# Kernel optimization log

Measured on AMD Instinct MI355X. Metric: run time of the kernel, lower is better.

Reference implementation:

```python
import jax, jax.numpy as jnp
import numpy as np

NUM_GROUPS = 32
EPS = 1e-6


def group_norm(x, gamma, beta):
    # x: [b, c, h, w]
    b, c, h, w = x.shape
    g = NUM_GROUPS
    xg = x.reshape(b, g, c // g, h, w)
    mean = xg.mean(axis=(2, 3, 4), keepdims=True)
    var = xg.var(axis=(2, 3, 4), keepdims=True)
    xn = ((xg - mean) * jax.lax.rsqrt(var + EPS)).reshape(b, c, h, w)
    return xn * gamma[None, :, None, None] + beta[None, :, None, None]


def conv1x1(x, w, b):
    # x: [b, c, h, w], w: [out_c, in_c], b: [out_c]
    return jnp.einsum('bchw,oc->bohw', x, w) + b[None, :, None, None]


def setup_inputs() -> dict:
    key = jax.random.key(0)
    ks = jax.random.split(key, 11)
    B, C, H, W = 4, 512, 64, 64
    s = 1.0 / np.sqrt(C)
    inp = {
        'x': jax.random.normal(ks[0], (B, C, H, W), dtype=jnp.float32),
        'gn_gamma': jnp.ones((C,), dtype=jnp.float32),
        'gn_beta': jnp.zeros((C,), dtype=jnp.float32),
        'wq': jax.random.normal(ks[1], (C, C), dtype=jnp.float32) * s,
        'bq': jax.random.normal(ks[2], (C,), dtype=jnp.float32) * 0.01,
        'wk': jax.random.normal(ks[3], (C, C), dtype=jnp.float32) * s,
        'bk': jax.random.normal(ks[4], (C,), dtype=jnp.float32) * 0.01,
        'wv': jax.random.normal(ks[5], (C, C), dtype=jnp.float32) * s,
        'bv': jax.random.normal(ks[6], (C,), dtype=jnp.float32) * 0.01,
        'wo': jax.random.normal(ks[7], (C, C), dtype=jnp.float32) * s,
        'bo': jax.random.normal(ks[8], (C,), dtype=jnp.float32) * 0.01,
    }
    return inp


def reference(x, gn_gamma, gn_beta, wq, bq, wk, bk, wv, bv, wo, bo):
    b, c, h, w = x.shape
    h_ = group_norm(x, gn_gamma, gn_beta)
    q = conv1x1(h_, wq, bq).reshape(b, c, h * w)  # [b, c, n]
    k = conv1x1(h_, wk, bk).reshape(b, c, h * w)
    v = conv1x1(h_, wv, bv).reshape(b, c, h * w)
    scale = jnp.asarray(c, x.dtype) ** -0.5
    # attn[b, i, j] = softmax_j(q_i . k_j * scale)
    attn = jax.nn.softmax(jnp.einsum('bci,bcj->bij', q, k) * scale, axis=-1)
    # A[b, c, i] = sum_j attn[b, i, j] * v[b, c, j]
    A = jnp.einsum('bij,bcj->bci', attn, v).reshape(b, c, h, w)
    A = conv1x1(A, wo, bo)
    # NOTE: the original module multiplies (not adds) the input by the attention output
    return x * A
```

## Files before the change

### kernel.cpp

```cpp
#include <hip/hip_runtime.h>
#include <hip/hip_bf16.h>
#include <stdint.h>

typedef __bf16 bf16x8 __attribute__((ext_vector_type(8)));
typedef __bf16 bf16x4 __attribute__((ext_vector_type(4)));
typedef float f32x4 __attribute__((ext_vector_type(4)));

__device__ __forceinline__ void gload_lds16(const __bf16* g, __bf16* l) {
  __builtin_amdgcn_global_load_lds(
      (const __attribute__((address_space(1))) void*)g,
      (__attribute__((address_space(3))) void*)l, 16, 0, 0);
}

__global__ __launch_bounds__(256) void cvt4_kernel(const float* __restrict__ s0,
                                                   const float* __restrict__ s1,
                                                   const float* __restrict__ s2,
                                                   const float* __restrict__ s3,
                                                   __bf16* __restrict__ dst) {
  int i = blockIdx.x * 256 + threadIdx.x;
  const float* srcs[4] = {s0, s1, s2, s3};
  int m = i >> 18;
  dst[i] = (__bf16)srcs[m][i & 262143];
}

__global__ __launch_bounds__(256) void biascat_kernel(const float* __restrict__ bq,
                                                      const float* __restrict__ bk,
                                                      float* __restrict__ bqk) {
  int i = blockIdx.x * 256 + threadIdx.x;
  bqk[i] = (i < 512) ? bq[i] : bk[i - 512];
}

__global__ __launch_bounds__(256) void gn1a_kernel(const float* __restrict__ x,
                                                   __bf16* __restrict__ xbf,
                                                   float2* __restrict__ part) {
  const int tid = threadIdx.x;
  const int s = blockIdx.x & 7;
  const int g = (blockIdx.x >> 3) & 31;
  const int b = blockIdx.x >> 8;
  const size_t base4 = (((size_t)b * 512 + g * 16) * 4096 + s * 8192) >> 2;
  const float4* x4 = (const float4*)x;
  bf16x4* o4 = (bf16x4*)xbf;

  float s1 = 0.f, s2 = 0.f;
#pragma unroll
  for (int j = 0; j < 8; ++j) {
    float4 t = x4[base4 + tid + j * 256];
    s1 += t.x + t.y + t.z + t.w;
    s2 += t.x * t.x + t.y * t.y + t.z * t.z + t.w * t.w;
    bf16x4 o;
    o[0] = (__bf16)t.x; o[1] = (__bf16)t.y; o[2] = (__bf16)t.z; o[3] = (__bf16)t.w;
    o4[base4 + tid + j * 256] = o;
  }
#pragma unroll
  for (int off = 32; off; off >>= 1) {
    s1 += __shfl_xor(s1, off);
    s2 += __shfl_xor(s2, off);
  }
  __shared__ float r1[4], r2[4];
  if ((tid & 63) == 0) { r1[tid >> 6] = s1; r2[tid >> 6] = s2; }
  __syncthreads();
  if (tid == 0)
    part[blockIdx.x] = float2{r1[0] + r1[1] + r1[2] + r1[3],
                              r2[0] + r2[1] + r2[2] + r2[3]};
}

__global__ __launch_bounds__(512) void gn1b_kernel(const float2* __restrict__ part,
                                                   const float* __restrict__ gamma,
                                                   const float* __restrict__ beta,
                                                   float2* __restrict__ gmbt) {
  const int b = blockIdx.x;
  const int t = threadIdx.x;
  __shared__ float sm[32], si[32];
  if (t < 32) {
    float s1 = 0.f, s2 = 0.f;
#pragma unroll
    for (int j = 0; j < 8; ++j) {
      float2 p = part[(b * 32 + t) * 8 + j];
      s1 += p.x; s2 += p.y;
    }
    const float mean = s1 * (1.f / 65536.f);
    const float var = s2 * (1.f / 65536.f) - mean * mean;
    sm[t] = mean;
    si[t] = rsqrtf(var + 1e-6f);
  }
  __syncthreads();
  const int g = t >> 4;
  const float gm = gamma[t] * si[g];
  gmbt[b * 512 + t] = float2{gm, beta[t] - sm[g] * gm};
}

__global__ __launch_bounds__(256) void gn2_kernel(const __bf16* __restrict__ xbf,
                                                  const float2* __restrict__ gmbt,
                                                  __bf16* __restrict__ hnT) {
  const int b = blockIdx.z;
  const int c0 = blockIdx.y * 64;
  const int n0 = blockIdx.x * 64;
  const int t = threadIdx.x;
  __shared__ __bf16 tile[64][72];

  {
    const int row = t >> 2;
    const int col = (t & 3) * 16;
    const __bf16* src = xbf + ((size_t)(b * 512 + c0 + row)) * 4096 + n0 + col;
    bf16x8 u0 = *(const bf16x8*)src;
    bf16x8 u1 = *(const bf16x8*)(src + 8);
    *(bf16x8*)&tile[row][col] = u0;
    *(bf16x8*)&tile[row][col + 8] = u1;
  }
  __syncthreads();
  {
    const int nrow = t >> 2;
    const int cc = (t & 3) * 16;
    bf16x8 o0, o1;
#pragma unroll
    for (int j = 0; j < 16; ++j) {
      const int c = c0 + cc + j;
      float2 s = gmbt[b * 512 + c];
      float val = (float)tile[cc + j][nrow] * s.x + s.y;
      if (j < 8) o0[j] = (__bf16)val; else o1[j - 8] = (__bf16)val;
    }
    __bf16* dst = hnT + ((size_t)b * 4096 + n0 + nrow) * 512 + c0 + cc;
    *(bf16x8*)dst = o0;
    *(bf16x8*)(dst + 8) = o1;
  }
}

__global__ __launch_bounds__(256) void softmax_bf16_kernel(__bf16* __restrict__ S) {
  const int N = 4096;
  __bf16* rp = S + (size_t)blockIdx.x * N;
  const int tid = threadIdx.x;
  bf16x8 v0 = ((const bf16x8*)rp)[tid * 2];
  bf16x8 v1 = ((const bf16x8*)rp)[tid * 2 + 1];
  float f[16];
#pragma unroll
  for (int i = 0; i < 8; ++i) { f[i] = (float)v0[i]; f[8 + i] = (float)v1[i]; }

  float mx = -1e30f;
#pragma unroll
  for (int i = 0; i < 16; ++i) mx = fmaxf(mx, f[i]);
#pragma unroll
  for (int off = 32; off; off >>= 1) mx = fmaxf(mx, __shfl_xor(mx, off));
  __shared__ float redm[4];
  if ((tid & 63) == 0) redm[tid >> 6] = mx;
  __syncthreads();
  mx = fmaxf(fmaxf(redm[0], redm[1]), fmaxf(redm[2], redm[3]));

  float sum = 0.f;
#pragma unroll
  for (int i = 0; i < 16; ++i) {
    f[i] = __expf(f[i] - mx);
    sum += f[i];
  }
#pragma unroll
  for (int off = 32; off; off >>= 1) sum += __shfl_xor(sum, off);
  __shared__ float reds[4];
  if ((tid & 63) == 0) reds[tid >> 6] = sum;
  __syncthreads();
  sum = reds[0] + reds[1] + reds[2] + reds[3];
  const float invs = 1.0f / sum;

  bf16x8 o0, o1;
#pragma unroll
  for (int i = 0; i < 8; ++i) {
    o0[i] = (__bf16)(f[i] * invs);
    o1[i] = (__bf16)(f[8 + i] * invs);
  }
  ((bf16x8*)rp)[tid * 2] = o0;
  ((bf16x8*)rp)[tid * 2 + 1] = o1;
}

template <int EPI, int BIAS>
__global__ __launch_bounds__(256) void gemm_lds_kernel(
    const __bf16* __restrict__ A, int lda, long long sA,
    const __bf16* __restrict__ Bm, int ldb, long long sB,
    void* __restrict__ Out, int ldo, long long sO,
    const float* __restrict__ bias, const __bf16* __restrict__ xmul,
    long long sX, float scale, int K) {
  __shared__ __bf16 sTa[2][128 * 32];
  __shared__ __bf16 sTb[2][128 * 32];

  const int gx = gridDim.x, gxy = gx * gridDim.y;
  const int nwg = gxy * gridDim.z;
  int bid = blockIdx.x + gx * blockIdx.y + gxy * blockIdx.z;
  if ((nwg & 7) == 0) bid = (bid & 7) * (nwg >> 3) + (bid >> 3);
  const int bz = bid / gxy;
  const int rem = bid - bz * gxy;
  const int by = rem / gx;
  const int bx = rem - by * gx;

  const int tid = threadIdx.x;
  const int lane = tid & 63;
  const int wid = tid >> 6;
  const int wr = wid >> 1, wc = wid & 1;
  const int tm0 = by * 128, tn0 = bx * 128;
  const int lr = lane & 15, lk = (lane >> 4) * 8;

  const int ch0 = wid * 2;
  const int srow = lane >> 2;
  const int scol = (lane & 3) * 8;
  const __bf16* gA0 = A + (size_t)bz * sA + (size_t)(tm0 + ch0 * 16 + srow) * lda + scol;
  const __bf16* gB0 = Bm + (size_t)bz * sB + (size_t)(tn0 + ch0 * 16 + srow) * ldb + scol;
  const size_t stepA = (size_t)16 * lda, stepB = (size_t)16 * ldb;

  f32x4 acc[4][4];
#pragma unroll
  for (int i = 0; i < 4; ++i)
#pragma unroll
    for (int j = 0; j < 4; ++j) acc[i][j] = f32x4{0.f, 0.f, 0.f, 0.f};

  const int T = K >> 5;
  gload_lds16(gA0, &sTa[0][ch0 * 512]);
  gload_lds16(gA0 + stepA, &sTa[0][ch0 * 512 + 512]);
  gload_lds16(gB0, &sTb[0][ch0 * 512]);
  gload_lds16(gB0 + stepB, &sTb[0][ch0 * 512 + 512]);

  for (int t = 0; t < T; ++t) {
    __syncthreads();
    const int cur = t & 1;
    if (t + 1 < T) {
      const __bf16* a = gA0 + (size_t)(t + 1) * 32;
      const __bf16* b = gB0 + (size_t)(t + 1) * 32;
      gload_lds16(a, &sTa[cur ^ 1][ch0 * 512]);
      gload_lds16(a + stepA, &sTa[cur ^ 1][ch0 * 512 + 512]);
      gload_lds16(b, &sTb[cur ^ 1][ch0 * 512]);
      gload_lds16(b + stepB, &sTb[cur ^ 1][ch0 * 512 + 512]);
    }
    const __bf16* fa = &sTa[cur][(wr * 64 + lr) * 32 + lk];
    const __bf16* fb = &sTb[cur][(wc * 64 + lr) * 32 + lk];
    bf16x8 a[4], b[4];
#pragma unroll
    for (int i = 0; i < 4; ++i) a[i] = *(const bf16x8*)(fa + i * 512);
#pragma unroll
    for (int j = 0; j < 4; ++j) b[j] = *(const bf16x8*)(fb + j * 512);
#pragma unroll
    for (int i = 0; i < 4; ++i)
#pragma unroll
      for (int j = 0; j < 4; ++j)
        acc[i][j] = __builtin_amdgcn_mfma_f32_16x16x32_bf16(a[i], b[j], acc[i][j], 0, 0, 0);
  }

  const int wm = tm0 + wr * 64, wn = tn0 + wc * 64;
#pragma unroll
  for (int i = 0; i < 4; ++i) {
#pragma unroll
    for (int r = 0; r < 4; ++r) {
      const int row = wm + i * 16 + (lane >> 4) * 4 + r;
#pragma unroll
      for (int j = 0; j < 4; ++j) {
        const int col = wn + j * 16 + lr;
        float val = acc[i][j][r] * scale;
        if (BIAS == 1) val += bias[col];
        if (BIAS == 2) val += bias[row];
        const size_t off = (size_t)bz * sO + (size_t)row * ldo + col;
        if (EPI == 0) {
          ((__bf16*)Out)[off] = (__bf16)val;
        } else if (EPI == 1) {
          ((float*)Out)[off] = val;
        } else {
          ((float*)Out)[off] = (float)xmul[(size_t)bz * sX + (size_t)row * ldo + col] * val;
        }
      }
    }
  }
}

extern "C" void kernel_launch(void* const* d_in, const int* in_sizes, int n_in,
                              void* d_out, int out_size, void* d_ws, size_t ws_size,
                              hipStream_t stream) {
  const int C = 512, N = 4096;
  const float* x = (const float*)d_in[0];
  const float* gng = (const float*)d_in[1];
  const float* gnb = (const float*)d_in[2];
  const float* wq = (const float*)d_in[3];
  const float* bq = (const float*)d_in[4];
  const float* wk = (const float*)d_in[5];
  const float* bk = (const float*)d_in[6];
  const float* wv = (const float*)d_in[7];
  const float* bv = (const float*)d_in[8];
  const float* wo = (const float*)d_in[9];
  const float* bo = (const float*)d_in[10];

  char* ws = (char*)d_ws;
  const size_t MB = 1ull << 20;
  const long long NC = (long long)N * C;
  const long long NN = (long long)N * N;
  const long long NQK = (long long)N * 1024;
  const bool batched = ws_size >= 194 * MB + 32768;

  __bf16 *S, *qkT, *a2T, *v, *xbf, *wqB;
  char* misc;
  if (batched) {
    S   = (__bf16*)(ws);
    qkT = (__bf16*)(ws + 128 * MB);
    a2T = qkT;
    v   = (__bf16*)(ws + 160 * MB);
    xbf = (__bf16*)(ws + 176 * MB);
    wqB = (__bf16*)(ws + 192 * MB);
    misc = ws + 194 * MB;
  } else {
    S   = (__bf16*)(ws);
    qkT = (__bf16*)(ws + 32 * MB);
    a2T = (__bf16*)(ws + 64 * MB);
    v   = (__bf16*)(ws + 80 * MB);
    xbf = (__bf16*)(ws + 96 * MB);
    wqB = (__bf16*)(ws + 112 * MB);
    misc = ws + 114 * MB;
  }
  __bf16* hnT = (__bf16*)ws;
  __bf16* wkB = wqB + 262144;
  __bf16* wvB = wkB + 262144;
  __bf16* woB = wvB + 262144;
  float* bqk   = (float*)misc;
  float2* gmbt = (float2*)(misc + 4096);
  float2* part = (float2*)(misc + 20480);

  const float scl = 0.044194173824159216f;

  cvt4_kernel<<<4096, 256, 0, stream>>>(wq, wk, wv, wo, wqB);
  biascat_kernel<<<4, 256, 0, stream>>>(bq, bk, bqk);
  gn1a_kernel<<<1024, 256, 0, stream>>>(x, xbf, part);
  gn1b_kernel<<<4, 512, 0, stream>>>(part, gng, gnb, gmbt);
  gn2_kernel<<<dim3(64, 8, 4), 256, 0, stream>>>(xbf, gmbt, hnT);

  gemm_lds_kernel<0, 1><<<dim3(8, 32, 4), 256, 0, stream>>>(
      hnT, C, NC, wqB, C, 0, qkT, 1024, NQK, bqk, nullptr, 0, 1.f, C);
  gemm_lds_kernel<0, 2><<<dim3(32, 4, 4), 256, 0, stream>>>(
      wvB, C, 0, hnT, C, NC, v, N, NC, bv, nullptr, 0, 1.f, C);

  if (batched) {
    gemm_lds_kernel<0, 0><<<dim3(32, 32, 4), 256, 0, stream>>>(
        qkT, 1024, NQK, qkT + 512, 1024, NQK, S, N, NN, nullptr, nullptr, 0, scl, C);
    softmax_bf16_kernel<<<4 * 4096, 256, 0, stream>>>(S);
    gemm_lds_kernel<0, 0><<<dim3(4, 32, 4), 256, 0, stream>>>(
        S, N, NN, v, N, NC, a2T, C, NC, nullptr, nullptr, 0, 1.f, N);
  } else {
    for (int b = 0; b < 4; ++b) {
      gemm_lds_kernel<0, 0><<<dim3(32, 32, 1), 256, 0, stream>>>(
          qkT + (size_t)b * NQK, 1024, 0, qkT + (size_t)b * NQK + 512, 1024, 0,
          S, N, 0, nullptr, nullptr, 0, scl, C);
      softmax_bf16_kernel<<<4096, 256, 0, stream>>>(S);
      gemm_lds_kernel<0, 0><<<dim3(4, 32, 1), 256, 0, stream>>>(
          S, N, 0, v + (size_t)b * NC, N, 0, a2T + (size_t)b * NC, C, 0,
          nullptr, nullptr, 0, 1.f, N);
    }
  }

  gemm_lds_kernel<2, 2><<<dim3(32, 4, 4), 256, 0, stream>>>(
      woB, C, 0, a2T, C, NC, d_out, N, NC, bo, xbf, NC, 1.f, C);
}
```

Before: 322.5 us.

## Add 256-row 8-wave GEMM with 4-slot LDS pipeline for QK, scores and PV

Adds a 512-thread GEMM kernel that computes 256xBN tiles. It uses a four-stage global-to-LDS ring with XOR-swizzled layout, explicit vmcnt waits, barrier-phased MFMA blocks and s_setprio. This kernel replaces the 128x128 double-buffered GEMM for the QK projection, the QK^T score GEMM and the attention-times-V GEMM, aiming for more reuse per LDS load and better overlap of loads with MFMA. It also simplifies the group-norm partial-sum indexing to a linear block offset. The cost is larger LDS use and tiles that assume K is a multiple of 128 and M a multiple of 256.

```diff
diff --git a/kernel.cpp b/kernel.cpp
--- a/kernel.cpp
+++ b/kernel.cpp
@@ -34,10 +34,7 @@
                                                    __bf16* __restrict__ xbf,
                                                    float2* __restrict__ part) {
   const int tid = threadIdx.x;
-  const int s = blockIdx.x & 7;
-  const int g = (blockIdx.x >> 3) & 31;
-  const int b = blockIdx.x >> 8;
-  const size_t base4 = (((size_t)b * 512 + g * 16) * 4096 + s * 8192) >> 2;
+  const size_t base4 = ((size_t)blockIdx.x * 8192) >> 2;
   const float4* x4 = (const float4*)x;
   bf16x4* o4 = (bf16x4*)xbf;
 
@@ -169,6 +166,143 @@
   ((bf16x8*)rp)[tid * 2 + 1] = o1;
 }
 
+template <int BN, int BIAS>
+__global__ __launch_bounds__(512) void gemm8p_kernel(
+    const __bf16* __restrict__ A, int lda, long long sA,
+    const __bf16* __restrict__ Bm, int ldb, long long sB,
+    __bf16* __restrict__ Out, int ldo, long long sO,
+    const float* __restrict__ bias, float scale, int K) {
+  constexpr int NF = BN / 64;
+  constexpr int NH = NF / 2;
+  constexpr int BSLOT = BN * 32;
+  __shared__ __bf16 sm[4 * 8192 + 4 * BSLOT];
+  __bf16* smB = sm + 4 * 8192;
+
+  const int gx = gridDim.x, gxy = gx * gridDim.y;
+  const int nwg = gxy * gridDim.z;
+  int bid = blockIdx.x + gx * blockIdx.y + gxy * blockIdx.z;
+  bid = (bid & 7) * (nwg >> 3) + (bid >> 3);
+  const int bz = bid / gxy;
+  const int rem = bid - bz * gxy;
+  const int by = rem / gx, bx = rem - by * gx;
+  const int tm0 = by * 256, tn0 = bx * BN;
+
+  const int t = threadIdx.x;
+  const int lane = t & 63, wid = t >> 6;
+  const int wr = wid >> 2, wc = wid & 3;
+
+  const __bf16* Az = A + (size_t)bz * sA;
+  const __bf16* Bz = Bm + (size_t)bz * sB;
+
+  const int scol = ((t & 3) * 8) ^ (((t >> 3) & 3) * 8);
+  const __bf16* gA0 = Az + (size_t)(tm0 + (t >> 2)) * lda + scol;
+  const __bf16* gA1 = gA0 + (size_t)128 * lda;
+  const __bf16* gB0 = Bz + (size_t)(tn0 + (t >> 2)) * ldb + scol;
+  const __bf16* gB1 = gB0 + (size_t)128 * ldb;
+  __bf16* dA = sm + t * 8;
+  __bf16* dB = smB + t * 8;
+
+  auto stageA = [&](int ko, int sl) {
+    gload_lds16(gA0 + ko, dA + sl * 8192);
+    gload_lds16(gA1 + ko, dA + sl * 8192 + 4096);
+  };
+  auto stageB = [&](int ko, int sl) {
+    gload_lds16(gB0 + ko, dB + sl * BSLOT);
+    if constexpr (BN == 256) gload_lds16(gB1 + ko, dB + sl * BSLOT + 4096);
+  };
+  auto vmw = [&] {
+    if constexpr (BN == 256) asm volatile("s_waitcnt vmcnt(8)" ::: "memory");
+    else                     asm volatile("s_waitcnt vmcnt(6)" ::: "memory");
+  };
+
+  const int lr = lane & 15;
+  const int kb = ((lane >> 4) * 16) ^ ((lr & 6) << 3);
+  const __bf16* rdA = sm + (((wr * 128 + lr) * 64 + kb) >> 1);
+  const __bf16* rdB = smB + (((wc * (BN / 4) + lr) * 64 + kb) >> 1);
+
+  f32x4 acc[8][NF];
+#pragma unroll
+  for (int m = 0; m < 8; ++m)
+#pragma unroll
+    for (int n = 0; n < NF; ++n) acc[m][n] = f32x4{0.f, 0.f, 0.f, 0.f};
+  bf16x8 av[8];
+
+  auto rdAfr = [&](int sl) {
+#pragma unroll
+    for (int m = 0; m < 8; ++m)
+      av[m] = *(const bf16x8*)(rdA + sl * 8192 + m * 512);
+  };
+  auto mmaPh = [&](int sl, int nh) {
+    bf16x8 bv[NH];
+#pragma unroll
+    for (int j = 0; j < NH; ++j)
+      bv[j] = *(const bf16x8*)(rdB + sl * BSLOT + (nh * NH + j) * 512);
+    __builtin_amdgcn_s_barrier();
+    __builtin_amdgcn_s_setprio(1);
+#pragma unroll
+    for (int m = 0; m < 8; ++m)
+#pragma unroll
+      for (int j = 0; j < NH; ++j)
+        acc[m][nh * NH + j] = __builtin_amdgcn_mfma_f32_16x16x32_bf16(
+            av[m], bv[j], acc[m][nh * NH + j], 0, 0, 0);
+    __builtin_amdgcn_s_setprio(0);
+    __builtin_amdgcn_s_barrier();
+  };
+
+  const int NT = K >> 6;
+  const int NIT = NT >> 1;
+
+  stageA(0, 0); stageB(0, 0); stageA(32, 1); stageB(32, 1);
+  stageA(64, 2); stageB(64, 2);
+  vmw();
+  __builtin_amdgcn_s_barrier();
+
+  for (int it = 0; it < NIT - 1; ++it) {
+    const int kt = it * 2;
+    const int k0 = kt * 64;
+    rdAfr(0); stageA(k0 + 96, 3);          mmaPh(0, 0);
+    stageB(k0 + 96, 3); vmw();             mmaPh(0, 1);
+    rdAfr(1); stageA(k0 + 128, 0);         mmaPh(1, 0);
+    stageB(k0 + 128, 0); vmw();            mmaPh(1, 1);
+    rdAfr(2); stageA(k0 + 160, 1);         mmaPh(2, 0);
+    stageB(k0 + 160, 1); vmw();            mmaPh(2, 1);
+    rdAfr(3); stageA(k0 + 192, 2);         mmaPh(3, 0);
+    stageB(k0 + 192, 2); vmw();            mmaPh(3, 1);
+  }
+  {
+    const int k0 = (NT - 2) * 64;
+    rdAfr(0); stageA(k0 + 96, 3);          mmaPh(0, 0);
+    stageB(k0 + 96, 3); vmw();             mmaPh(0, 1);
+    rdAfr(1);                              mmaPh(1, 0);
+    if constexpr (BN == 256) asm volatile("s_waitcnt vmcnt(4)" ::: "memory");
+    else                     asm volatile("s_waitcnt vmcnt(3)" ::: "memory");
+    mmaPh(1, 1);
+    rdAfr(2);                              mmaPh(2, 0);
+    if constexpr (BN == 256) asm volatile("s_waitcnt vmcnt(2)" ::: "memory");
+    else                     asm volatile("s_waitcnt vmcnt(1)" ::: "memory");
+    mmaPh(2, 1);
+    rdAfr(3);                              mmaPh(3, 0);
+    mmaPh(3, 1);
+  }
+
+  const int q4 = (lane >> 4) * 4;
+  const int wnb = tn0 + wc * (BN / 4);
+  float bcol[NF];
+#pragma unroll
+  for (int n = 0; n < NF; ++n) bcol[n] = BIAS ? bias[wnb + n * 16 + lr] : 0.f;
+#pragma unroll
+  for (int m = 0; m < 8; ++m) {
+#pragma unroll
+    for (int r = 0; r < 4; ++r) {
+      const int row = tm0 + wr * 128 + m * 16 + q4 + r;
+      __bf16* orow = Out + (size_t)bz * sO + (size_t)row * ldo + wnb + lr;
+#pragma unroll
+      for (int n = 0; n < NF; ++n)
+        orow[n * 16] = (__bf16)(acc[m][n][r] * scale + bcol[n]);
+    }
+  }
+}
+
 template <int EPI, int BIAS>
 __global__ __launch_bounds__(256) void gemm_lds_kernel(
     const __bf16* __restrict__ A, int lda, long long sA,
@@ -214,12 +348,12 @@
   gload_lds16(gB0, &sTb[0][ch0 * 512]);
   gload_lds16(gB0 + stepB, &sTb[0][ch0 * 512 + 512]);
 
-  for (int t = 0; t < T; ++t) {
+  for (int tt = 0; tt < T; ++tt) {
     __syncthreads();
-    const int cur = t & 1;
-    if (t + 1 < T) {
-      const __bf16* a = gA0 + (size_t)(t + 1) * 32;
-      const __bf16* b = gB0 + (size_t)(t + 1) * 32;
+    const int cur = tt & 1;
+    if (tt + 1 < T) {
+      const __bf16* a = gA0 + (size_t)(tt + 1) * 32;
+      const __bf16* b = gB0 + (size_t)(tt + 1) * 32;
       gload_lds16(a, &sTa[cur ^ 1][ch0 * 512]);
       gload_lds16(a + stepA, &sTa[cur ^ 1][ch0 * 512 + 512]);
       gload_lds16(b, &sTb[cur ^ 1][ch0 * 512]);
@@ -307,8 +441,7 @@
     misc = ws + 114 * MB;
   }
   __bf16* hnT = (__bf16*)ws;
-  __bf16* wkB = wqB + 262144;
-  __bf16* wvB = wkB + 262144;
+  __bf16* wvB = wqB + 2 * 262144;
   __bf16* woB = wvB + 262144;
   float* bqk   = (float*)misc;
   float2* gmbt = (float2*)(misc + 4096);
@@ -322,29 +455,29 @@
   gn1b_kernel<<<4, 512, 0, stream>>>(part, gng, gnb, gmbt);
   gn2_kernel<<<dim3(64, 8, 4), 256, 0, stream>>>(xbf, gmbt, hnT);
 
-  gemm_lds_kernel<0, 1><<<dim3(8, 32, 4), 256, 0, stream>>>(
-      hnT, C, NC, wqB, C, 0, qkT, 1024, NQK, bqk, nullptr, 0, 1.f, C);
+  gemm8p_kernel<256, 1><<<dim3(4, 16, 4), 512, 0, stream>>>(
+      hnT, C, NC, wqB, C, 0, qkT, 1024, NQK, bqk, 1.f, C);
   gemm_lds_kernel<0, 2><<<dim3(32, 4, 4), 256, 0, stream>>>(
       wvB, C, 0, hnT, C, NC, v, N, NC, bv, nullptr, 0, 1.f, C);
 
   if (batched) {
-    gemm_lds_kernel<0, 0><<<dim3(32, 32, 4), 256, 0, stream>>>(
-        qkT, 1024, NQK, qkT + 512, 1024, NQK, S, N, NN, nullptr, nullptr, 0, scl, C);
+    gemm8p_kernel<256, 0><<<dim3(16, 16, 4), 512, 0, stream>>>(
+        qkT, 1024, NQK, qkT + 512, 1024, NQK, S, N, NN, nullptr, scl, C);
     softmax_bf16_kernel<<<4 * 4096, 256, 0, stream>>>(S);
-    gemm_lds_kernel<0, 0><<<dim3(4, 32, 4), 256, 0, stream>>>(
-        S, N, NN, v, N, NC, a2T, C, NC, nullptr, nullptr, 0, 1.f, N);
+    gemm8p_kernel<128, 0><<<dim3(4, 16, 4), 512, 0, stream>>>(
+        S, N, NN, v, N, NC, a2T, C, NC, nullptr, 1.f, N);
   } else {
     for (int b = 0; b < 4; ++b) {
-      gemm_lds_kernel<0, 0><<<dim3(32, 32, 1), 256, 0, stream>>>(
+      gemm8p_kernel<256, 0><<<dim3(16, 16, 1), 512, 0, stream>>>(
           qkT + (size_t)b * NQK, 1024, 0, qkT + (size_t)b * NQK + 512, 1024, 0,
-          S, N, 0, nullptr, nullptr, 0, scl, C);
+          S, N, 0, nullptr, scl, C);
       softmax_bf16_kernel<<<4096, 256, 0, stream>>>(S);
-      gemm_lds_kernel<0, 0><<<dim3(4, 32, 1), 256, 0, stream>>>(
+      gemm8p_kernel<128, 0><<<dim3(4, 16, 1), 512, 0, stream>>>(
           S, N, 0, v + (size_t)b * NC, N, 0, a2T + (size_t)b * NC, C, 0,
-          nullptr, nullptr, 0, 1.f, N);
+          nullptr, 1.f, N);
     }
   }
 
   gemm_lds_kernel<2, 2><<<dim3(32, 4, 4), 256, 0, stream>>>(
-      woB, C, 0, a2T, C, NC, d_out, N, NC, bo, xbf, NC, 1.f, C);
-}
+      woB, C, 0, a2T, C, NC, (float*)d_out, N, NC, bo, xbf, NC, 1.f, C);
+}
```

Measured after the change: 292.7 us. 1.1x faster.
